# Optimization experiments

Hardware: AMD Instinct MI355X
Metric: run time of the kernel (lower is better)

The kernel has to match this reference:

```python
import jax, jax.numpy as jnp
import numpy as np

B = 16384       # batch
G = 8           # groups
S = 16          # state_c (per-group in/out channels)
H = 512         # hidden_c (per-group hidden channels)
FACTOR = 1.0
SWISH_DIV = 1.1


def setup_inputs() -> dict:
    key = jax.random.key(0)
    ks = jax.random.split(key, 12)
    def w(k, shape, fan_in):
        bound = 1.0 / np.sqrt(fan_in)
        return jax.random.uniform(k, shape, jnp.float32, -bound, bound)
    return {
        "x":  jax.random.normal(ks[0], (B, G * S), dtype=jnp.float32),
        # grouped 1x1 convs as per-group linear weights [G, out_c, in_c]
        "W1": w(ks[1], (G, H, S), S), "b1": w(ks[2], (G, H), S),
        "beta1": jnp.full((G,), 0.5, jnp.float32),
        "W2": w(ks[3], (G, H, H), H), "b2": w(ks[4], (G, H), H),
        "beta2": jnp.full((G,), 0.5, jnp.float32),
        "W3": w(ks[5], (G, H, H), H), "b3": w(ks[6], (G, H), H),
        "beta3": jnp.full((G,), 0.5, jnp.float32),
        "W4": w(ks[7], (G, S, H), H), "b4": w(ks[8], (G, S), H),
    }


def _group_swish(x, beta):
    # x: [B, G, C]; beta: [G] -> y = x * sigmoid(x * softplus(beta)) / 1.1
    sp = jax.nn.softplus(beta)[None, :, None]
    return x * jax.nn.sigmoid(x * sp) / SWISH_DIV


def reference(x, W1, b1, beta1, W2, b2, beta2, W3, b3, beta3, W4, b4):
    h = x.reshape(-1, G, S)                                   # [B,G,S]
    h = jnp.einsum('bgs,ghs->bgh', h, W1) + b1[None]          # [B,G,H]
    h = _group_swish(h, beta1)
    h = jnp.einsum('bgi,goi->bgo', h, W2) + b2[None]
    h = _group_swish(h, beta2)
    h = jnp.einsum('bgi,goi->bgo', h, W3) + b3[None]
    h = _group_swish(h, beta3)
    h = jnp.einsum('bgh,gsh->bgs', h, W4) + b4[None]          # [B,G,S]
    return h.reshape(-1, G * S) * FACTOR
```

## Files before the change

kernel.cpp:

```cpp
#include <hip/hip_runtime.h>
#include <stdint.h>

#define G_ 8
#define S_ 16
#define H_ 512
#define TB 64
#define NTH 512

typedef _Float16 h16;
typedef _Float16 h16x8 __attribute__((ext_vector_type(8)));
typedef float f32x4 __attribute__((ext_vector_type(4)));

#define XB_STRIDE 40
#define HB_BYTES (TB * 1024)
#define SMEM_BYTES (HB_BYTES + TB * XB_STRIDE * 2)

__device__ __forceinline__ float swishf(float v, float sp) {
    const float e = __expf(-v * sp);
    return v * __builtin_amdgcn_rcpf(1.0f + e) * (1.0f / 1.1f);
}

__device__ __forceinline__ uint32_t hswz(int row, uint32_t byte_in_row) {
    return (uint32_t)row * 1024u + (byte_in_row ^ (((uint32_t)(row & 7)) << 4));
}

template<bool USEWS>
__device__ __forceinline__ h16x8 loadBfrag(const h16* __restrict__ wpk,
                                           const float* __restrict__ wf,
                                           int colBlk, int k0, int ln, int K, int Ksrc) {
    if constexpr (USEWS) {
        return *(const h16x8*)(wpk + ((size_t)colBlk * (K >> 5) + (k0 >> 5)) * 512 + ln * 8);
    } else {
        const int row = colBlk * 16 + (ln & 15);
        const int k = k0 + (ln >> 4) * 8;
        h16x8 r;
        if (k < Ksrc) {
            const float* p = wf + (size_t)row * Ksrc + k;
            #pragma unroll
            for (int j = 0; j < 8; ++j) r[j] = (h16)p[j];
        } else {
            #pragma unroll
            for (int j = 0; j < 8; ++j) r[j] = (h16)0.f;
        }
        return r;
    }
}

__device__ __forceinline__ void swish_store(const f32x4 (&acc)[4][4], char* hb,
                                            const float* __restrict__ bias, float sp,
                                            int wc0, int ln) {
    const int l15 = ln & 15, lq = ln >> 4, pe = l15 & 1;
    #pragma unroll
    for (int nt = 0; nt < 4; ++nt) {
        const int col = wc0 + nt * 16 + l15;
        const float bv = bias[col];
        const uint32_t cb2 = (uint32_t)((col & ~1) * 2);
        #pragma unroll
        for (int mt = 0; mt < 4; ++mt) {
            float v[4], t[4];
            #pragma unroll
            for (int r = 0; r < 4; ++r) v[r] = swishf(acc[mt][nt][r] + bv, sp);
            #pragma unroll
            for (int r = 0; r < 4; ++r) t[r] = __shfl_xor(v[r], 1);
            const int rowb = mt * 16 + lq * 4 + 2 * pe;
            #pragma unroll
            for (int q = 0; q < 2; ++q) {
                const float a0 = pe ? t[2 + q] : v[q];
                const float a1 = pe ? v[2 + q] : t[q];
                union { h16 h[2]; uint32_t u; } pk;
                pk.h[0] = (h16)a0; pk.h[1] = (h16)a1;
                *(uint32_t*)(hb + hswz(rowb + q, cb2)) = pk.u;
            }
        }
    }
}

template<bool USEWS>
__device__ __forceinline__ void layerH(f32x4 (&acc)[4][4],
                                       const h16* __restrict__ wpk, const float* __restrict__ wf,
                                       const char* __restrict__ hb, int wc0, int ln) {
    const int l15 = ln & 15, lq = ln >> 4;
    const int cB = wc0 >> 4;
    #pragma unroll
    for (int mt = 0; mt < 4; ++mt)
        #pragma unroll
        for (int nt = 0; nt < 4; ++nt) acc[mt][nt] = (f32x4){0.f, 0.f, 0.f, 0.f};

    h16x8 bfr[4];
    #pragma unroll
    for (int nt = 0; nt < 4; ++nt)
        bfr[nt] = loadBfrag<USEWS>(wpk, wf, cB + nt, 0, ln, H_, H_);

    #pragma unroll 2
    for (int k0 = 0; k0 < H_; k0 += 32) {
        h16x8 bnx[4];
        const int kn = (k0 + 32 < H_) ? (k0 + 32) : 0;
        #pragma unroll
        for (int nt = 0; nt < 4; ++nt)
            bnx[nt] = loadBfrag<USEWS>(wpk, wf, cB + nt, kn, ln, H_, H_);
        #pragma unroll
        for (int mt = 0; mt < 4; ++mt) {
            const h16x8 a = *(const h16x8*)(hb + hswz(mt * 16 + l15,
                                                      (uint32_t)(k0 * 2 + lq * 16)));
            #pragma unroll
            for (int nt = 0; nt < 4; ++nt)
                acc[mt][nt] = __builtin_amdgcn_mfma_f32_16x16x32_f16(a, bfr[nt], acc[mt][nt], 0, 0, 0);
        }
        #pragma unroll
        for (int nt = 0; nt < 4; ++nt) bfr[nt] = bnx[nt];
    }
}

template<bool USEWS>
__global__ __launch_bounds__(NTH, 4) void mlp_fused(
    const float* __restrict__ x,
    const float* __restrict__ W1f, const float* __restrict__ b1, const float* __restrict__ be1,
    const float* __restrict__ W2f, const float* __restrict__ b2, const float* __restrict__ be2,
    const float* __restrict__ W3f, const float* __restrict__ b3, const float* __restrict__ be3,
    const float* __restrict__ W4f, const float* __restrict__ b4,
    const h16* __restrict__ W1p, const h16* __restrict__ W2p,
    const h16* __restrict__ W3p, const h16* __restrict__ W4p,
    float* __restrict__ out) {
    extern __shared__ char smem[];
    h16* __restrict__ xb = (h16*)(smem + HB_BYTES);

    const int bid = blockIdx.x;
    const int g = bid & 7;
    const int rowbase = (bid >> 3) * TB;
    const int tid = threadIdx.x;
    const int wv = tid >> 6;
    const int ln = tid & 63;
    const int l15 = ln & 15;
    const int lq = ln >> 4;
    const int wc0 = wv * 64;

    const float sp1 = log1pf(__expf(be1[g]));
    const float sp2 = log1pf(__expf(be2[g]));
    const float sp3 = log1pf(__expf(be3[g]));

    const h16* w1p = W1p + (size_t)g * H_ * 32;
    const h16* w2p = W2p + (size_t)g * H_ * H_;
    const h16* w3p = W3p + (size_t)g * H_ * H_;
    const h16* w4p = W4p + (size_t)g * S_ * H_;
    const float* w1f = W1f + (size_t)g * H_ * S_;
    const float* w2f = W2f + (size_t)g * H_ * H_;
    const float* w3f = W3f + (size_t)g * H_ * H_;
    const float* w4f = W4f + (size_t)g * S_ * H_;

    for (int i = tid; i < TB * S_; i += NTH) {
        const int r = i >> 4, s = i & 15;
        const float v = x[(size_t)(rowbase + r) * (G_ * S_) + g * S_ + s];
        xb[r * XB_STRIDE + s] = (h16)v;
        xb[r * XB_STRIDE + 16 + s] = (h16)0.f;
    }
    __syncthreads();

    f32x4 acc[4][4];

    {
        #pragma unroll
        for (int mt = 0; mt < 4; ++mt)
            #pragma unroll
            for (int nt = 0; nt < 4; ++nt) acc[mt][nt] = (f32x4){0.f, 0.f, 0.f, 0.f};
        h16x8 bfr[4];
        #pragma unroll
        for (int nt = 0; nt < 4; ++nt)
            bfr[nt] = loadBfrag<USEWS>(w1p, w1f, (wc0 >> 4) + nt, 0, ln, 32, S_);
        #pragma unroll
        for (int mt = 0; mt < 4; ++mt) {
            const h16x8 a = *(const h16x8*)(xb + (mt * 16 + l15) * XB_STRIDE + lq * 8);
            #pragma unroll
            for (int nt = 0; nt < 4; ++nt)
                acc[mt][nt] = __builtin_amdgcn_mfma_f32_16x16x32_f16(a, bfr[nt], acc[mt][nt], 0, 0, 0);
        }
    }
    swish_store(acc, smem, b1 + g * H_, sp1, wc0, ln);
    __syncthreads();

    layerH<USEWS>(acc, w2p, w2f, smem, wc0, ln);
    __syncthreads();
    swish_store(acc, smem, b2 + g * H_, sp2, wc0, ln);
    __syncthreads();

    layerH<USEWS>(acc, w3p, w3f, smem, wc0, ln);
    __syncthreads();
    swish_store(acc, smem, b3 + g * H_, sp3, wc0, ln);
    __syncthreads();

    if (wv < 4) {
        f32x4 a4 = {0.f, 0.f, 0.f, 0.f};
        #pragma unroll 2
        for (int k0 = 0; k0 < H_; k0 += 32) {
            const h16x8 a = *(const h16x8*)(smem + hswz(wv * 16 + l15,
                                                        (uint32_t)(k0 * 2 + lq * 16)));
            const h16x8 b = loadBfrag<USEWS>(w4p, w4f, 0, k0, ln, H_, H_);
            a4 = __builtin_amdgcn_mfma_f32_16x16x32_f16(a, b, a4, 0, 0, 0);
        }
        const float bv = b4[g * S_ + l15];
        #pragma unroll
        for (int r = 0; r < 4; ++r)
            out[(size_t)(rowbase + wv * 16 + lq * 4 + r) * (G_ * S_) + g * S_ + l15] = a4[r] + bv;
    }
}

__global__ void packW(const float* __restrict__ s, h16* __restrict__ d,
                      int N, int Kd, int Ks) {
    const int t = blockIdx.x * 256 + threadIdx.x;
    const int total = (N * Kd) >> 3;
    if (t >= total) return;
    const int ln = t & 63;
    const int blk = t >> 6;
    const int kblocks = Kd >> 5;
    const int kb = blk % kblocks;
    const int nb = blk / kblocks;
    const int row = nb * 16 + (ln & 15);
    const int k = kb * 32 + (ln >> 4) * 8;
    h16x8 o;
    #pragma unroll
    for (int j = 0; j < 8; ++j)
        o[j] = (h16)((k + j < Ks) ? s[(size_t)row * Ks + k + j] : 0.f);
    *(h16x8*)(d + (size_t)t * 8) = o;
}

extern "C" void kernel_launch(void* const* d_in, const int* in_sizes, int n_in,
                              void* d_out, int out_size, void* d_ws, size_t ws_size,
                              hipStream_t stream) {
    const float* x   = (const float*)d_in[0];
    const float* W1  = (const float*)d_in[1];
    const float* b1  = (const float*)d_in[2];
    const float* be1 = (const float*)d_in[3];
    const float* W2  = (const float*)d_in[4];
    const float* b2  = (const float*)d_in[5];
    const float* be2 = (const float*)d_in[6];
    const float* W3  = (const float*)d_in[7];
    const float* b3  = (const float*)d_in[8];
    const float* be3 = (const float*)d_in[9];
    const float* W4  = (const float*)d_in[10];
    const float* b4  = (const float*)d_in[11];
    float* out = (float*)d_out;

    const size_t nW2  = (size_t)G_ * H_ * H_;
    const size_t nW1p = (size_t)G_ * H_ * 32;
    const size_t nW4  = (size_t)G_ * S_ * H_;
    const size_t need = (2 * nW2 + nW1p + nW4) * sizeof(h16);

    const dim3 grid(2048), blk(NTH);

    if (ws_size >= need) {
        h16* W2p = (h16*)d_ws;
        h16* W3p = W2p + nW2;
        h16* W1p = W3p + nW2;
        h16* W4p = W1p + nW1p;
        packW<<<dim3((unsigned)((nW2 / 8 + 255) / 256)), dim3(256), 0, stream>>>(W2, W2p, G_ * H_, H_, H_);
        packW<<<dim3((unsigned)((nW2 / 8 + 255) / 256)), dim3(256), 0, stream>>>(W3, W3p, G_ * H_, H_, H_);
        packW<<<dim3((unsigned)((nW4 / 8 + 255) / 256)), dim3(256), 0, stream>>>(W4, W4p, G_ * S_, H_, H_);
        packW<<<dim3((unsigned)((nW1p / 8 + 255) / 256)), dim3(256), 0, stream>>>(W1, W1p, G_ * H_, 32, S_);
        (void)hipFuncSetAttribute(reinterpret_cast<const void*>(mlp_fused<true>),
                                  hipFuncAttributeMaxDynamicSharedMemorySize, (int)SMEM_BYTES);
        mlp_fused<true><<<grid, blk, SMEM_BYTES, stream>>>(
            x, W1, b1, be1, W2, b2, be2, W3, b3, be3, W4, b4,
            W1p, W2p, W3p, W4p, out);
    } else {
        (void)hipFuncSetAttribute(reinterpret_cast<const void*>(mlp_fused<false>),
                                  hipFuncAttributeMaxDynamicSharedMemorySize, (int)SMEM_BYTES);
        mlp_fused<false><<<grid, blk, SMEM_BYTES, stream>>>(
            x, W1, b1, be1, W2, b2, be2, W3, b3, be3, W4, b4,
            nullptr, nullptr, nullptr, nullptr, out);
    }
}
```

Measured before the change: 208.7 us.

## Switch hidden layers to 32x32x16 MFMA with swapped operand roles and deeper prefetch

Replaces the 16x16x32 MFMA tiling with 32x32x16 MFMAs in which the weights are the A operand and the activations the B operand. This transposes the accumulator layout so the swish epilogue can write four packed halfs per store with no lane shuffles. It also adds a two-step-ahead weight prefetch, one-step-ahead LDS prefetch and s_setprio around the MFMA bursts. Weight packing is reworked to match, W1 is no longer zero-padded to K=32, and x loads and output stores are vectorised. The larger fragments and extra prefetch registers raise register pressure and risk lower occupancy.

```diff
diff --git a/kernel.cpp b/kernel.cpp
--- a/kernel.cpp
+++ b/kernel.cpp
@@ -10,8 +10,9 @@
 typedef _Float16 h16;
 typedef _Float16 h16x8 __attribute__((ext_vector_type(8)));
 typedef float f32x4 __attribute__((ext_vector_type(4)));
-
-#define XB_STRIDE 40
+typedef float f32x16 __attribute__((ext_vector_type(16)));
+
+#define XB_STRIDE 24
 #define HB_BYTES (TB * 1024)
 #define SMEM_BYTES (HB_BYTES + TB * XB_STRIDE * 2)
 
@@ -20,94 +21,118 @@
     return v * __builtin_amdgcn_rcpf(1.0f + e) * (1.0f / 1.1f);
 }
 
+__device__ __forceinline__ uint32_t pk16(float a, float b) {
+    return __builtin_bit_cast(uint32_t, __builtin_amdgcn_cvt_pkrtz(a, b));
+}
+
 __device__ __forceinline__ uint32_t hswz(int row, uint32_t byte_in_row) {
     return (uint32_t)row * 1024u + (byte_in_row ^ (((uint32_t)(row & 7)) << 4));
 }
 
 template<bool USEWS>
-__device__ __forceinline__ h16x8 loadBfrag(const h16* __restrict__ wpk,
-                                           const float* __restrict__ wf,
-                                           int colBlk, int k0, int ln, int K, int Ksrc) {
+__device__ __forceinline__ h16x8 loadA32(const h16* __restrict__ wpk,
+                                         const float* __restrict__ wf,
+                                         int nb, int ks, int ln, int KB, int Ksrc) {
     if constexpr (USEWS) {
-        return *(const h16x8*)(wpk + ((size_t)colBlk * (K >> 5) + (k0 >> 5)) * 512 + ln * 8);
+        return *(const h16x8*)(wpk + (((size_t)nb * KB + ks) * 64 + ln) * 8);
     } else {
-        const int row = colBlk * 16 + (ln & 15);
-        const int k = k0 + (ln >> 4) * 8;
+        const int row = nb * 32 + (ln & 31);
+        const int k = ks * 16 + (ln >> 5) * 8;
+        const float* p = wf + (size_t)row * Ksrc + k;
         h16x8 r;
-        if (k < Ksrc) {
-            const float* p = wf + (size_t)row * Ksrc + k;
+        #pragma unroll
+        for (int j = 0; j < 8; ++j) r[j] = (h16)p[j];
+        return r;
+    }
+}
+
+template<bool USEWS>
+__device__ __forceinline__ h16x8 loadA16(const h16* __restrict__ wpk,
+                                         const float* __restrict__ wf,
+                                         int ks32, int ln, int Ksrc) {
+    if constexpr (USEWS) {
+        return *(const h16x8*)(wpk + ((size_t)ks32 * 64 + ln) * 8);
+    } else {
+        const int row = ln & 15;
+        const int k = ks32 * 32 + (ln >> 4) * 8;
+        const float* p = wf + (size_t)row * Ksrc + k;
+        h16x8 r;
+        #pragma unroll
+        for (int j = 0; j < 8; ++j) r[j] = (h16)p[j];
+        return r;
+    }
+}
+
+__device__ __forceinline__ void swish_store32(const f32x16 (&acc)[2][2], char* hb,
+                                              const float* __restrict__ bias, float sp,
+                                              int wc0, int ln) {
+    const int l31 = ln & 31, lh = ln >> 5;
+    #pragma unroll
+    for (int ot = 0; ot < 2; ++ot) {
+        #pragma unroll
+        for (int rq = 0; rq < 4; ++rq) {
+            const int col0 = wc0 + ot * 32 + rq * 8 + lh * 4;
+            const f32x4 bv = *(const f32x4*)(bias + col0);
             #pragma unroll
-            for (int j = 0; j < 8; ++j) r[j] = (h16)p[j];
-        } else {
-            #pragma unroll
-            for (int j = 0; j < 8; ++j) r[j] = (h16)0.f;
-        }
-        return r;
-    }
-}
-
-__device__ __forceinline__ void swish_store(const f32x4 (&acc)[4][4], char* hb,
-                                            const float* __restrict__ bias, float sp,
-                                            int wc0, int ln) {
-    const int l15 = ln & 15, lq = ln >> 4, pe = l15 & 1;
-    #pragma unroll
-    for (int nt = 0; nt < 4; ++nt) {
-        const int col = wc0 + nt * 16 + l15;
-        const float bv = bias[col];
-        const uint32_t cb2 = (uint32_t)((col & ~1) * 2);
-        #pragma unroll
-        for (int mt = 0; mt < 4; ++mt) {
-            float v[4], t[4];
-            #pragma unroll
-            for (int r = 0; r < 4; ++r) v[r] = swishf(acc[mt][nt][r] + bv, sp);
-            #pragma unroll
-            for (int r = 0; r < 4; ++r) t[r] = __shfl_xor(v[r], 1);
-            const int rowb = mt * 16 + lq * 4 + 2 * pe;
-            #pragma unroll
-            for (int q = 0; q < 2; ++q) {
-                const float a0 = pe ? t[2 + q] : v[q];
-                const float a1 = pe ? v[2 + q] : t[q];
-                union { h16 h[2]; uint32_t u; } pk;
-                pk.h[0] = (h16)a0; pk.h[1] = (h16)a1;
-                *(uint32_t*)(hb + hswz(rowb + q, cb2)) = pk.u;
+            for (int bt = 0; bt < 2; ++bt) {
+                const int b = bt * 32 + l31;
+                const float v0 = swishf(acc[ot][bt][rq * 4 + 0] + bv[0], sp);
+                const float v1 = swishf(acc[ot][bt][rq * 4 + 1] + bv[1], sp);
+                const float v2 = swishf(acc[ot][bt][rq * 4 + 2] + bv[2], sp);
+                const float v3 = swishf(acc[ot][bt][rq * 4 + 3] + bv[3], sp);
+                const uint64_t u = (uint64_t)pk16(v0, v1)
+                                 | ((uint64_t)pk16(v2, v3) << 32);
+                *(uint64_t*)(hb + hswz(b, (uint32_t)(col0 * 2))) = u;
             }
         }
     }
 }
 
 template<bool USEWS>
-__device__ __forceinline__ void layerH(f32x4 (&acc)[4][4],
-                                       const h16* __restrict__ wpk, const float* __restrict__ wf,
-                                       const char* __restrict__ hb, int wc0, int ln) {
-    const int l15 = ln & 15, lq = ln >> 4;
-    const int cB = wc0 >> 4;
-    #pragma unroll
-    for (int mt = 0; mt < 4; ++mt)
-        #pragma unroll
-        for (int nt = 0; nt < 4; ++nt) acc[mt][nt] = (f32x4){0.f, 0.f, 0.f, 0.f};
-
-    h16x8 bfr[4];
-    #pragma unroll
-    for (int nt = 0; nt < 4; ++nt)
-        bfr[nt] = loadBfrag<USEWS>(wpk, wf, cB + nt, 0, ln, H_, H_);
-
-    #pragma unroll 2
-    for (int k0 = 0; k0 < H_; k0 += 32) {
-        h16x8 bnx[4];
-        const int kn = (k0 + 32 < H_) ? (k0 + 32) : 0;
-        #pragma unroll
-        for (int nt = 0; nt < 4; ++nt)
-            bnx[nt] = loadBfrag<USEWS>(wpk, wf, cB + nt, kn, ln, H_, H_);
-        #pragma unroll
-        for (int mt = 0; mt < 4; ++mt) {
-            const h16x8 a = *(const h16x8*)(hb + hswz(mt * 16 + l15,
-                                                      (uint32_t)(k0 * 2 + lq * 16)));
+__device__ __forceinline__ void layerH32(f32x16 (&acc)[2][2],
+                                         const h16* __restrict__ wpk, const float* __restrict__ wf,
+                                         const char* __restrict__ hb, int wc0, int ln) {
+    const int l31 = ln & 31, lh = ln >> 5;
+    const int cB = wc0 >> 5;
+    #pragma unroll
+    for (int ot = 0; ot < 2; ++ot)
+        #pragma unroll
+        for (int bt = 0; bt < 2; ++bt) acc[ot][bt] = (f32x16)(0.f);
+
+    h16x8 aC[2], aN[2], bC[2];
+    #pragma unroll
+    for (int ot = 0; ot < 2; ++ot) {
+        aC[ot] = loadA32<USEWS>(wpk, wf, cB + ot, 0, ln, 32, H_);
+        aN[ot] = loadA32<USEWS>(wpk, wf, cB + ot, 1, ln, 32, H_);
+    }
+    #pragma unroll
+    for (int bt = 0; bt < 2; ++bt)
+        bC[bt] = *(const h16x8*)(hb + hswz(bt * 32 + l31, (uint32_t)(lh * 16)));
+
+    #pragma unroll 4
+    for (int ks = 0; ks < 32; ++ks) {
+        h16x8 aF[2], bN[2];
+        const int ksA = (ks + 2 < 32) ? ks + 2 : 0;
+        const int ksB = (ks + 1 < 32) ? ks + 1 : 0;
+        #pragma unroll
+        for (int ot = 0; ot < 2; ++ot)
+            aF[ot] = loadA32<USEWS>(wpk, wf, cB + ot, ksA, ln, 32, H_);
+        #pragma unroll
+        for (int bt = 0; bt < 2; ++bt)
+            bN[bt] = *(const h16x8*)(hb + hswz(bt * 32 + l31,
+                                               (uint32_t)(ksB * 32 + lh * 16)));
+        __builtin_amdgcn_s_setprio(1);
+        #pragma unroll
+        for (int ot = 0; ot < 2; ++ot)
             #pragma unroll
-            for (int nt = 0; nt < 4; ++nt)
-                acc[mt][nt] = __builtin_amdgcn_mfma_f32_16x16x32_f16(a, bfr[nt], acc[mt][nt], 0, 0, 0);
-        }
-        #pragma unroll
-        for (int nt = 0; nt < 4; ++nt) bfr[nt] = bnx[nt];
+            for (int bt = 0; bt < 2; ++bt)
+                acc[ot][bt] = __builtin_amdgcn_mfma_f32_32x32x16_f16(aC[ot], bC[bt],
+                                                                     acc[ot][bt], 0, 0, 0);
+        __builtin_amdgcn_s_setprio(0);
+        #pragma unroll
+        for (int ot = 0; ot < 2; ++ot) { aC[ot] = aN[ot]; aN[ot] = aF[ot]; }
+        #pragma unroll
+        for (int bt = 0; bt < 2; ++bt) bC[bt] = bN[bt];
     }
 }
 
@@ -130,15 +155,15 @@
     const int tid = threadIdx.x;
     const int wv = tid >> 6;
     const int ln = tid & 63;
-    const int l15 = ln & 15;
-    const int lq = ln >> 4;
+    const int l31 = ln & 31;
+    const int lh = ln >> 5;
     const int wc0 = wv * 64;
 
     const float sp1 = log1pf(__expf(be1[g]));
     const float sp2 = log1pf(__expf(be2[g]));
     const float sp3 = log1pf(__expf(be3[g]));
 
-    const h16* w1p = W1p + (size_t)g * H_ * 32;
+    const h16* w1p = W1p + (size_t)g * H_ * S_;
     const h16* w2p = W2p + (size_t)g * H_ * H_;
     const h16* w3p = W3p + (size_t)g * H_ * H_;
     const h16* w4p = W4p + (size_t)g * S_ * H_;
@@ -147,78 +172,101 @@
     const float* w3f = W3f + (size_t)g * H_ * H_;
     const float* w4f = W4f + (size_t)g * S_ * H_;
 
-    for (int i = tid; i < TB * S_; i += NTH) {
-        const int r = i >> 4, s = i & 15;
-        const float v = x[(size_t)(rowbase + r) * (G_ * S_) + g * S_ + s];
-        xb[r * XB_STRIDE + s] = (h16)v;
-        xb[r * XB_STRIDE + 16 + s] = (h16)0.f;
-    }
-    __syncthreads();
-
-    f32x4 acc[4][4];
-
     {
-        #pragma unroll
-        for (int mt = 0; mt < 4; ++mt)
+        const int idx = tid * 2;
+        const int r = idx >> 4, s = idx & 15;
+        const float2 v = *(const float2*)(x + (size_t)(rowbase + r) * (G_ * S_) + g * S_ + s);
+        *(uint32_t*)((char*)xb + (r * XB_STRIDE + s) * 2) = pk16(v.x, v.y);
+    }
+    __syncthreads();
+
+    f32x16 acc[2][2];
+
+    {
+        #pragma unroll
+        for (int ot = 0; ot < 2; ++ot)
             #pragma unroll
-            for (int nt = 0; nt < 4; ++nt) acc[mt][nt] = (f32x4){0.f, 0.f, 0.f, 0.f};
-        h16x8 bfr[4];
-        #pragma unroll
-        for (int nt = 0; nt < 4; ++nt)
-            bfr[nt] = loadBfrag<USEWS>(w1p, w1f, (wc0 >> 4) + nt, 0, ln, 32, S_);
-        #pragma unroll
-        for (int mt = 0; mt < 4; ++mt) {
-            const h16x8 a = *(const h16x8*)(xb + (mt * 16 + l15) * XB_STRIDE + lq * 8);
+            for (int bt = 0; bt < 2; ++bt) acc[ot][bt] = (f32x16)(0.f);
+        h16x8 aW[2], bX[2];
+        #pragma unroll
+        for (int ot = 0; ot < 2; ++ot)
+            aW[ot] = loadA32<USEWS>(w1p, w1f, (wc0 >> 5) + ot, 0, ln, 1, S_);
+        #pragma unroll
+        for (int bt = 0; bt < 2; ++bt)
+            bX[bt] = *(const h16x8*)(xb + (bt * 32 + l31) * XB_STRIDE + lh * 8);
+        #pragma unroll
+        for (int ot = 0; ot < 2; ++ot)
             #pragma unroll
-            for (int nt = 0; nt < 4; ++nt)
-                acc[mt][nt] = __builtin_amdgcn_mfma_f32_16x16x32_f16(a, bfr[nt], acc[mt][nt], 0, 0, 0);
-        }
-    }
-    swish_store(acc, smem, b1 + g * H_, sp1, wc0, ln);
-    __syncthreads();
-
-    layerH<USEWS>(acc, w2p, w2f, smem, wc0, ln);
-    __syncthreads();
-    swish_store(acc, smem, b2 + g * H_, sp2, wc0, ln);
-    __syncthreads();
-
-    layerH<USEWS>(acc, w3p, w3f, smem, wc0, ln);
-    __syncthreads();
-    swish_store(acc, smem, b3 + g * H_, sp3, wc0, ln);
+            for (int bt = 0; bt < 2; ++bt)
+                acc[ot][bt] = __builtin_amdgcn_mfma_f32_32x32x16_f16(aW[ot], bX[bt],
+                                                                     acc[ot][bt], 0, 0, 0);
+    }
+    swish_store32(acc, smem, b1 + g * H_, sp1, wc0, ln);
+    __syncthreads();
+
+    layerH32<USEWS>(acc, w2p, w2f, smem, wc0, ln);
+    __syncthreads();
+    swish_store32(acc, smem, b2 + g * H_, sp2, wc0, ln);
+    __syncthreads();
+
+    layerH32<USEWS>(acc, w3p, w3f, smem, wc0, ln);
+    __syncthreads();
+    swish_store32(acc, smem, b3 + g * H_, sp3, wc0, ln);
     __syncthreads();
 
     if (wv < 4) {
         f32x4 a4 = {0.f, 0.f, 0.f, 0.f};
-        #pragma unroll 2
-        for (int k0 = 0; k0 < H_; k0 += 32) {
-            const h16x8 a = *(const h16x8*)(smem + hswz(wv * 16 + l15,
-                                                        (uint32_t)(k0 * 2 + lq * 16)));
-            const h16x8 b = loadBfrag<USEWS>(w4p, w4f, 0, k0, ln, H_, H_);
+        const int l15 = ln & 15, lq = ln >> 4;
+        #pragma unroll 4
+        for (int ks = 0; ks < 16; ++ks) {
+            const h16x8 a = loadA16<USEWS>(w4p, w4f, ks, ln, H_);
+            const h16x8 b = *(const h16x8*)(smem + hswz(wv * 16 + l15,
+                                                        (uint32_t)(ks * 64 + lq * 16)));
             a4 = __builtin_amdgcn_mfma_f32_16x16x32_f16(a, b, a4, 0, 0, 0);
         }
-        const float bv = b4[g * S_ + l15];
-        #pragma unroll
-        for (int r = 0; r < 4; ++r)
-            out[(size_t)(rowbase + wv * 16 + lq * 4 + r) * (G_ * S_) + g * S_ + l15] = a4[r] + bv;
-    }
-}
-
-__global__ void packW(const float* __restrict__ s, h16* __restrict__ d,
-                      int N, int Kd, int Ks) {
+        const int brow = wv * 16 + l15;
+        const int s0 = lq * 4;
+        const f32x4 bv = *(const f32x4*)(b4 + g * S_ + s0);
+        f32x4 o4;
+        #pragma unroll
+        for (int r = 0; r < 4; ++r) o4[r] = a4[r] + bv[r];
+        *(f32x4*)(out + (size_t)(rowbase + brow) * (G_ * S_) + g * S_ + s0) = o4;
+    }
+}
+
+__global__ void packW32(const float* __restrict__ s, h16* __restrict__ d,
+                        int NB_total, int KB, int Ks) {
     const int t = blockIdx.x * 256 + threadIdx.x;
-    const int total = (N * Kd) >> 3;
+    const int total = NB_total * KB * 64;
     if (t >= total) return;
     const int ln = t & 63;
     const int blk = t >> 6;
-    const int kblocks = Kd >> 5;
-    const int kb = blk % kblocks;
-    const int nb = blk / kblocks;
-    const int row = nb * 16 + (ln & 15);
+    const int kb = blk % KB;
+    const int nbg = blk / KB;
+    const int row = nbg * 32 + (ln & 31);
+    const int k = kb * 16 + (ln >> 5) * 8;
+    const float* p = s + (size_t)row * Ks + k;
+    h16x8 o;
+    #pragma unroll
+    for (int j = 0; j < 8; ++j) o[j] = (h16)p[j];
+    *(h16x8*)(d + (size_t)t * 8) = o;
+}
+
+__global__ void packW16(const float* __restrict__ s, h16* __restrict__ d,
+                        int NB_total, int KB, int Ks) {
+    const int t = blockIdx.x * 256 + threadIdx.x;
+    const int total = NB_total * KB * 64;
+    if (t >= total) return;
+    const int ln = t & 63;
+    const int blk = t >> 6;
+    const int kb = blk % KB;
+    const int nbg = blk / KB;
+    const int row = nbg * 16 + (ln & 15);
     const int k = kb * 32 + (ln >> 4) * 8;
+    const float* p = s + (size_t)row * Ks + k;
     h16x8 o;
     #pragma unroll
-    for (int j = 0; j < 8; ++j)
-        o[j] = (h16)((k + j < Ks) ? s[(size_t)row * Ks + k + j] : 0.f);
+    for (int j = 0; j < 8; ++j) o[j] = (h16)p[j];
     *(h16x8*)(d + (size_t)t * 8) = o;
 }
 
@@ -240,7 +288,7 @@
     float* out = (float*)d_out;
 
     const size_t nW2  = (size_t)G_ * H_ * H_;
-    const size_t nW1p = (size_t)G_ * H_ * 32;
+    const size_t nW1p = (size_t)G_ * H_ * S_;
     const size_t nW4  = (size_t)G_ * S_ * H_;
     const size_t need = (2 * nW2 + nW1p + nW4) * sizeof(h16);
 
@@ -251,10 +299,10 @@
         h16* W3p = W2p + nW2;
         h16* W1p = W3p + nW2;
         h16* W4p = W1p + nW1p;
-        packW<<<dim3((unsigned)((nW2 / 8 + 255) / 256)), dim3(256), 0, stream>>>(W2, W2p, G_ * H_, H_, H_);
-        packW<<<dim3((unsigned)((nW2 / 8 + 255) / 256)), dim3(256), 0, stream>>>(W3, W3p, G_ * H_, H_, H_);
-        packW<<<dim3((unsigned)((nW4 / 8 + 255) / 256)), dim3(256), 0, stream>>>(W4, W4p, G_ * S_, H_, H_);
-        packW<<<dim3((unsigned)((nW1p / 8 + 255) / 256)), dim3(256), 0, stream>>>(W1, W1p, G_ * H_, 32, S_);
+        packW32<<<dim3((unsigned)((nW2 / 8 + 255) / 256)), dim3(256), 0, stream>>>(W2, W2p, G_ * 16, 32, H_);
+        packW32<<<dim3((unsigned)((nW2 / 8 + 255) / 256)), dim3(256), 0, stream>>>(W3, W3p, G_ * 16, 32, H_);
+        packW32<<<dim3((unsigned)((nW1p / 8 + 255) / 256)), dim3(256), 0, stream>>>(W1, W1p, G_ * 16, 1, S_);
+        packW16<<<dim3((unsigned)((nW4 / 8 + 255) / 256)), dim3(256), 0, stream>>>(W4, W4p, G_, 16, H_);
         (void)hipFuncSetAttribute(reinterpret_cast<const void*>(mlp_fused<true>),
                                   hipFuncAttributeMaxDynamicSharedMemorySize, (int)SMEM_BYTES);
         mlp_fused<true><<<grid, blk, SMEM_BYTES, stream>>>(
```

Result: no change. 205.9 us (-1.4%).
